# Performance work log

Hardware: AMD Instinct MI355X
Metric: run time of the kernel (lower is better)

## Reference

```python
import jax, jax.numpy as jnp
import numpy as np

N_QUBITS = 14      # must be even (module assert)
IN_CHANNEL = 512   # batch of independent circuits

# PennyLane convention: wire 0 is the most-significant bit of the basis index.

def _mcx_perm(n, c1, c2, t):
    # MultiControlledX with control_values '10': flip target bit t when bit(c1)==1 and bit(c2)==0
    idx = np.arange(2 ** n)
    b1 = (idx >> (n - 1 - c1)) & 1
    b2 = (idx >> (n - 1 - c2)) & 1
    return np.where((b1 == 1) & (b2 == 0), idx ^ (1 << (n - 1 - t)), idx)

_MCX_PERMS = [jnp.asarray(_mcx_perm(N_QUBITS, w, (w + 1) % N_QUBITS, (w + 2) % N_QUBITS))
              for w in range(N_QUBITS)]
# Z-eigenvalue signs per basis state per wire: (2^n, n)
_Z_SIGNS = jnp.asarray(
    np.stack([1.0 - 2.0 * ((np.arange(2 ** N_QUBITS) >> (N_QUBITS - 1 - w)) & 1)
              for w in range(N_QUBITS)], axis=1), dtype=jnp.float32)


def _apply_rx(state, theta, w):
    # RX(theta) = [[cos(t/2), -i sin(t/2)], [-i sin(t/2), cos(t/2)]] on wire w; theta: (B,)
    B = state.shape[0]
    st = state.reshape(B, 2 ** w, 2, -1)
    c = jnp.cos(0.5 * theta)[:, None, None]
    s = (-1j * jnp.sin(0.5 * theta))[:, None, None]
    s0, s1 = st[:, :, 0, :], st[:, :, 1, :]
    out = jnp.stack([c * s0 + s * s1, c * s1 + s * s0], axis=2)
    return out.reshape(B, -1)


def _apply_rz(state, theta, w):
    # RZ(theta) = diag(e^{-i t/2}, e^{+i t/2}) on wire w
    B = state.shape[0]
    st = state.reshape(B, 2 ** w, 2, -1)
    p0 = jnp.exp(-0.5j * theta)[:, None, None]
    p1 = jnp.exp(0.5j * theta)[:, None, None]
    out = jnp.stack([p0 * st[:, :, 0, :], p1 * st[:, :, 1, :]], axis=2)
    return out.reshape(B, -1)


def _apply_isingxx(state, phi, wa, wb):
    a, b = min(wa, wb), max(wa, wb)
    B = state.shape[0]
    st = state.reshape(B, 2 ** a, 2, 2 ** (b - a - 1), 2, -1)
    c = jnp.cos(0.5 * phi)[:, None, None, None]
    s = (-1j * jnp.sin(0.5 * phi))[:, None, None, None]
    s00 = st[:, :, 0, :, 0, :]; s01 = st[:, :, 0, :, 1, :]
    s10 = st[:, :, 1, :, 0, :]; s11 = st[:, :, 1, :, 1, :]
    row0 = jnp.stack([c * s00 + s * s11, c * s01 + s * s10], axis=3)  # (B, 2^a, M, 2, R)
    row1 = jnp.stack([c * s10 + s * s01, c * s11 + s * s00], axis=3)
    return jnp.stack([row0, row1], axis=2).reshape(B, -1)


def _circuit(cp, p):
    n = N_QUBITS
    B = cp.shape[0]
    state = jnp.zeros((B, 2 ** n), dtype=jnp.complex64).at[:, 0].set(1.0)
    for w in range(n):
        state = _apply_rx(state, p[:, 0, w], w)
    for ws in range(n // 2):
        state = _apply_isingxx(state, cp[:, ws], 2 * ws, 2 * ws + 1)
    for w in range(n):
        state = _apply_rz(state, p[:, 1, w], w)
    for ws in range(n // 2):
        wss = 2 * ws + 1
        state = _apply_isingxx(state, cp[:, ws + n // 2], wss, (wss + 1) % n)
    for w in range(n):
        state = _apply_rx(state, p[:, 2, w], w)
    for w in range(n):
        state = state[:, _MCX_PERMS[w]]
    probs = state.real ** 2 + state.imag ** 2  # (B, 2^n)
    return (probs @ _Z_SIGNS).astype(jnp.float32)  # (B, n) = expval PauliZ per wire


def setup_inputs() -> dict:
    key = jax.random.key(0)
    k1, k2 = jax.random.split(key)
    cp = jax.random.uniform(k1, (IN_CHANNEL, N_QUBITS), dtype=jnp.float32) * jnp.pi
    p = jax.random.uniform(k2, (IN_CHANNEL, 3, N_QUBITS), dtype=jnp.float32) * jnp.pi
    return {"cp": cp, "p": p}


def reference(cp, p):
    return _circuit(cp, p)
```

## Files before the change

kernel.cpp:

```cpp
#include <hip/hip_runtime.h>

#define NQ 14
#define NSTATE (1 << NQ)

typedef float  f2  __attribute__((ext_vector_type(2)));
typedef __fp16 h2v __attribute__((ext_vector_type(2)));

#define OFF_BTAB  (NSTATE*4)
#define OFF_RX3   (OFF_BTAB + 28*8)
#define OFF_XX2   (OFF_RX3 + 28*4)
#define OFF_RED   (OFF_XX2 + 14*4)
#define SMEM_BYTES (OFF_RED + 16*NQ*4)

__device__ __forceinline__ f2 cmul(f2 a, f2 b){
    f2 br = {-b.y, b.x};
    return a.x * b + a.y * br;
}

__device__ __forceinline__ void rot2(f2& A, f2& B, float c, float sn){
    f2 a = A, b = B;
    f2 ar = {a.y, -a.x};
    f2 br = {b.y, -b.x};
    A = c * a + sn * br;
    B = c * b + sn * ar;
}

__device__ __forceinline__ h2v pack(f2 v){ return __builtin_amdgcn_cvt_pkrtz(v.x, v.y); }
__device__ __forceinline__ f2  unpack(h2v h){ return (f2){(float)h.x, (float)h.y}; }

__device__ __forceinline__ int slotof(int i){ return i ^ ((i >> 5) & 31); }

__device__ __forceinline__ void gates16(f2 amp[16], float c0, float s0, float c1, float s1,
                                        const float* rc, const float* rs, int w0)
{
    #pragma unroll
    for (int lo = 0; lo < 4; ++lo) { rot2(amp[lo], amp[lo|12], c0, s0); rot2(amp[lo|4], amp[lo|8], c0, s0); }
    #pragma unroll
    for (int hi = 0; hi < 16; hi += 4) { rot2(amp[hi], amp[hi|3], c1, s1); rot2(amp[hi|1], amp[hi|2], c1, s1); }
    #pragma unroll
    for (int j = 0; j < 4; ++j) {
        const int bm = 1 << (3 - j);
        const float c = rc[w0 + j], s = rs[w0 + j];
        #pragma unroll
        for (int L = 0; L < 16; ++L)
            if (!(L & bm)) rot2(amp[L], amp[L | bm], c, s);
    }
}

__global__ void perm_tbl_kernel(unsigned short* __restrict__ tbl)
{
    const int i = blockIdx.x * blockDim.x + threadIdx.x;
    int x = i;
    #pragma unroll
    for (int w = 13; w >= 0; --w) {
        const int p1 = 13 - w;
        const int p2 = 13 - ((w + 1) % NQ);
        const int pt = 13 - ((w + 2) % NQ);
        const int cond = ((x >> p1) & ~(x >> p2)) & 1;
        x ^= cond << pt;
    }
    const int slot = x ^ ((x >> 5) & 31);
    tbl[(i & 1023) * 16 + (i >> 10)] = (unsigned short)slot;
}

__global__ void __launch_bounds__(1024, 8)
qsim_kernel(const float* __restrict__ cp, const float* __restrict__ p,
            const unsigned short* __restrict__ tbl, float* __restrict__ out)
{
    extern __shared__ __align__(16) char smem[];
    h2v* st    = reinterpret_cast<h2v*>(smem);
    f2*  Btab  = reinterpret_cast<f2*>(smem + OFF_BTAB);
    float* rx3c = reinterpret_cast<float*>(smem + OFF_RX3);
    float* rx3s = rx3c + 14;
    float* xx2c = reinterpret_cast<float*>(smem + OFF_XX2);
    float* xx2s = xx2c + 7;
    float* red  = reinterpret_cast<float*>(smem + OFF_RED);

    const int b = blockIdx.x;
    const int t = threadIdx.x;
    const float* pb  = p  + b * 42;
    const float* cpb = cp + b * 14;

    if (t < 7) {
        const int ws = t, wa = 2*ws, wb = 2*ws + 1;
        float sa, ca; sincosf(0.5f * pb[wa], &sa, &ca);
        float sb, cb; sincosf(0.5f * pb[wb], &sb, &cb);
        f2 s00 = {ca*cb, 0.f};
        f2 s01 = {0.f, -ca*sb};
        f2 s10 = {0.f, -sa*cb};
        f2 s11 = {-sa*sb, 0.f};
        float sx, cx; sincosf(0.5f * cpb[ws], &sx, &cx);
        rot2(s00, s11, cx, sx);
        rot2(s01, s10, cx, sx);
        const float ga = 0.5f * pb[14 + wa], gb = 0.5f * pb[14 + wb];
        float sA, cA; sincosf(ga + gb, &sA, &cA);
        float sB, cB; sincosf(gb - ga, &sB, &cB);
        s00 = cmul(s00, (f2){cA, -sA});
        s11 = cmul(s11, (f2){cA,  sA});
        s01 = cmul(s01, (f2){cB,  sB});
        s10 = cmul(s10, (f2){cB, -sB});
        const int k = 6 - ws;
        Btab[k*4+0] = s00; Btab[k*4+1] = s01; Btab[k*4+2] = s10; Btab[k*4+3] = s11;
    } else if (t >= 64 && t < 78) {
        const int w = t - 64;
        float s, c; sincosf(0.5f * pb[28 + w], &s, &c);
        rx3c[w] = c; rx3s[w] = s;
    } else if (t >= 128 && t < 135) {
        const int g = t - 128;
        float s, c; sincosf(0.5f * cpb[7 + g], &s, &c);
        xx2c[g] = c; xx2s[g] = s;
    }
    __syncthreads();

    f2 amp[16];

    {
        const int ibase = (t & 0x1FF) | ((t >> 9) << 13);
        f2 Pc = cmul(cmul(Btab[(ibase & 3)],            Btab[4  + ((ibase >> 2) & 3)]),
                     cmul(Btab[8 + ((ibase >> 4) & 3)], Btab[12 + ((ibase >> 6) & 3)]));
        const int b8  = (ibase >> 8) & 1;
        const int b13 = (ibase >> 13) & 1;
        #pragma unroll
        for (int L = 0; L < 16; ++L) {
            const int c4 = ((L & 1) << 1) | b8;
            const int c5 = (L >> 1) & 3;
            const int c6 = (b13 << 1) | ((L >> 3) & 1);
            amp[L] = cmul(cmul(Pc, Btab[16 + c4]), cmul(Btab[20 + c5], Btab[24 + c6]));
        }
        gates16(amp, xx2c[0], xx2s[0], xx2c[1], xx2s[1], rx3c, rx3s, 1);
        #pragma unroll
        for (int L = 0; L < 16; ++L) st[slotof(ibase | (L << 9))] = pack(amp[L]);
    }
    __syncthreads();

    {
        const int ibase = (t & 31) | ((t >> 5) << 9);
        #pragma unroll
        for (int L = 0; L < 16; ++L) amp[L] = unpack(st[slotof(ibase | (L << 5))]);
        gates16(amp, xx2c[2], xx2s[2], xx2c[3], xx2s[3], rx3c, rx3s, 5);
        #pragma unroll
        for (int L = 0; L < 16; ++L) st[slotof(ibase | (L << 5))] = pack(amp[L]);
    }
    __syncthreads();

    {
        const int ibase = (t & 1) | ((t >> 1) << 5);
        #pragma unroll
        for (int L = 0; L < 16; ++L) amp[L] = unpack(st[slotof(ibase | (L << 1))]);
        gates16(amp, xx2c[4], xx2s[4], xx2c[5], xx2s[5], rx3c, rx3s, 9);
        #pragma unroll
        for (int L = 0; L < 16; ++L) st[slotof(ibase | (L << 1))] = pack(amp[L]);
    }
    __syncthreads();

    {
        const int tb = t << 3;
        #pragma unroll
        for (int L = 0; L < 16; ++L) {
            const int i = tb | (L & 1) | (((L >> 1) & 1) << 13) | (((L >> 2) & 1) << 1) | (((L >> 3) & 1) << 2);
            amp[L] = unpack(st[slotof(i)]);
        }
        {
            const float c = xx2c[6], s = xx2s[6];
            #pragma unroll
            for (int f = 0; f < 16; f += 4) { rot2(amp[f], amp[f|3], c, s); rot2(amp[f|1], amp[f|2], c, s); }
        }
        {
            const float c = rx3c[13], s = rx3s[13];
            #pragma unroll
            for (int L = 0; L < 16; ++L) if (!(L & 1)) rot2(amp[L], amp[L|1], c, s);
        }
        {
            const float c = rx3c[0], s = rx3s[0];
            #pragma unroll
            for (int L = 0; L < 16; ++L) if (!(L & 2)) rot2(amp[L], amp[L|2], c, s);
        }
        #pragma unroll
        for (int L = 0; L < 16; ++L) {
            const int i = tb | (L & 1) | (((L >> 1) & 1) << 13) | (((L >> 2) & 1) << 1) | (((L >> 3) & 1) << 2);
            st[slotof(i)] = pack(amp[L]);
        }
    }
    __syncthreads();

    {
        unsigned off[16];
        {
            const uint4* tp = reinterpret_cast<const uint4*>(tbl + t * 16);
            const uint4 w0 = tp[0], w1 = tp[1];
            off[0]=w0.x&0xffffu; off[1]=w0.x>>16; off[2]=w0.y&0xffffu; off[3]=w0.y>>16;
            off[4]=w0.z&0xffffu; off[5]=w0.z>>16; off[6]=w0.w&0xffffu; off[7]=w0.w>>16;
            off[8]=w1.x&0xffffu; off[9]=w1.x>>16; off[10]=w1.y&0xffffu; off[11]=w1.y>>16;
            off[12]=w1.z&0xffffu; off[13]=w1.z>>16; off[14]=w1.w&0xffffu; off[15]=w1.w>>16;
        }
        float T = 0.f, U0 = 0.f, U1 = 0.f, U2 = 0.f, U3 = 0.f;
        #pragma unroll
        for (int k = 0; k < 16; ++k) {
            const f2 a = unpack(st[off[k]]);
            const float q = fmaf(a.x, a.x, a.y * a.y);
            T += q;
            if (k & 1) U0 += q;
            if (k & 2) U1 += q;
            if (k & 4) U2 += q;
            if (k & 8) U3 += q;
        }
        float s = T;
        float d0, d1, d2, d3, d4, d5;
        {
            float o;
            o = __shfl_xor(s, 1);  d0 = s - o; s += o;
            o = __shfl_xor(d0, 2); d0 += o;
            o = __shfl_xor(s, 2);  d1 = s - o; s += o;
            o = __shfl_xor(d0, 4); d0 += o;
            o = __shfl_xor(d1, 4); d1 += o;
            o = __shfl_xor(s, 4);  d2 = s - o; s += o;
            o = __shfl_xor(d0, 8); d0 += o;
            o = __shfl_xor(d1, 8); d1 += o;
            o = __shfl_xor(d2, 8); d2 += o;
            o = __shfl_xor(s, 8);  d3 = s - o; s += o;
            o = __shfl_xor(d0, 16); d0 += o;
            o = __shfl_xor(d1, 16); d1 += o;
            o = __shfl_xor(d2, 16); d2 += o;
            o = __shfl_xor(d3, 16); d3 += o;
            o = __shfl_xor(s, 16);  d4 = s - o; s += o;
            o = __shfl_xor(d0, 32); d0 += o;
            o = __shfl_xor(d1, 32); d1 += o;
            o = __shfl_xor(d2, 32); d2 += o;
            o = __shfl_xor(d3, 32); d3 += o;
            o = __shfl_xor(d4, 32); d4 += o;
            o = __shfl_xor(s, 32);  d5 = s - o; s += o;
        }
        #pragma unroll
        for (int m = 1; m < 64; m <<= 1) {
            U0 += __shfl_xor(U0, m);
            U1 += __shfl_xor(U1, m);
            U2 += __shfl_xor(U2, m);
            U3 += __shfl_xor(U3, m);
        }
        if ((t & 63) == 0) {
            const int v = t >> 6;
            float* r = red + v * NQ;
            r[0]  = s - 2.f * U3;
            r[1]  = s - 2.f * U2;
            r[2]  = s - 2.f * U1;
            r[3]  = s - 2.f * U0;
            r[4]  = (v & 8) ? -s : s;
            r[5]  = (v & 4) ? -s : s;
            r[6]  = (v & 2) ? -s : s;
            r[7]  = (v & 1) ? -s : s;
            r[8]  = d5;
            r[9]  = d4;
            r[10] = d3;
            r[11] = d2;
            r[12] = d1;
            r[13] = d0;
        }
    }
    __syncthreads();
    if (t < NQ) {
        float ssum = 0.f;
        #pragma unroll
        for (int wv = 0; wv < 16; ++wv) ssum += red[wv * NQ + t];
        out[b * NQ + t] = ssum;
    }
}

extern "C" void kernel_launch(void* const* d_in, const int* in_sizes, int n_in,
                              void* d_out, int out_size, void* d_ws, size_t ws_size,
                              hipStream_t stream)
{
    (void)n_in; (void)out_size; (void)ws_size;
    const float* cp = (const float*)d_in[0];
    const float* p  = (const float*)d_in[1];
    float* out = (float*)d_out;
    unsigned short* tbl = (unsigned short*)d_ws;
    const int B = in_sizes[0] / NQ;

    perm_tbl_kernel<<<NSTATE / 256, 256, 0, stream>>>(tbl);

    (void)hipFuncSetAttribute(reinterpret_cast<const void*>(qsim_kernel),
                              hipFuncAttributeMaxDynamicSharedMemorySize, SMEM_BYTES);
    qsim_kernel<<<B, 1024, SMEM_BYTES, stream>>>(cp, p, tbl, out);
}
```

Before: 89.28 us.

## Scatter final stage through forward MCX permutation into padded rows, read contiguously

Replaces the gather through the inverse MCX permutation in the reduction with a forward scatter. The last gate stage now writes each amplitude directly to its permuted position in a padded layout (row stride 72 bytes). This lets each thread read its 16 output amplitudes as 8 contiguous 4-half vectors and drops the separate store-then-gather pass. The table kernel now computes the forward permutation indexed by thread and register, and the shared-memory footprint grows by 8 KB for padding. An extra barrier is added before the scatter, and the reduction's wire-to-output mapping is reordered to match the new layout.

```diff
diff --git a/kernel.cpp b/kernel.cpp
--- a/kernel.cpp
+++ b/kernel.cpp
@@ -5,8 +5,9 @@
 
 typedef float  f2  __attribute__((ext_vector_type(2)));
 typedef __fp16 h2v __attribute__((ext_vector_type(2)));
-
-#define OFF_BTAB  (NSTATE*4)
+typedef __fp16 h4v __attribute__((ext_vector_type(4)));
+
+#define OFF_BTAB  (NSTATE*4 + 1024*8)
 #define OFF_RX3   (OFF_BTAB + 28*8)
 #define OFF_XX2   (OFF_RX3 + 28*4)
 #define OFF_RED   (OFF_XX2 + 14*4)
@@ -47,25 +48,26 @@
     }
 }
 
-__global__ void perm_tbl_kernel(unsigned short* __restrict__ tbl)
-{
-    const int i = blockIdx.x * blockDim.x + threadIdx.x;
-    int x = i;
-    #pragma unroll
-    for (int w = 13; w >= 0; --w) {
+__global__ void perm_tbl_kernel(unsigned short* __restrict__ tblD)
+{
+    const int j = blockIdx.x * blockDim.x + threadIdx.x;
+    int x = j;
+    #pragma unroll
+    for (int w = 0; w < NQ; ++w) {
         const int p1 = 13 - w;
         const int p2 = 13 - ((w + 1) % NQ);
         const int pt = 13 - ((w + 2) % NQ);
         const int cond = ((x >> p1) & ~(x >> p2)) & 1;
         x ^= cond << pt;
     }
-    const int slot = x ^ ((x >> 5) & 31);
-    tbl[(i & 1023) * 16 + (i >> 10)] = (unsigned short)slot;
+    const int t = (j >> 3) & 0x3FF;
+    const int L = (j & 1) | (((j >> 13) & 1) << 1) | (((j >> 1) & 1) << 2) | (((j >> 2) & 1) << 3);
+    tblD[t * 16 + L] = (unsigned short)x;
 }
 
 __global__ void __launch_bounds__(1024, 8)
 qsim_kernel(const float* __restrict__ cp, const float* __restrict__ p,
-            const unsigned short* __restrict__ tbl, float* __restrict__ out)
+            const unsigned short* __restrict__ tblD, float* __restrict__ out)
 {
     extern __shared__ __align__(16) char smem[];
     h2v* st    = reinterpret_cast<h2v*>(smem);
@@ -154,6 +156,9 @@
     __syncthreads();
 
     {
+        const uint4* tp = reinterpret_cast<const uint4*>(tblD + t * 16);
+        const uint4 w0 = tp[0], w1 = tp[1];
+
         const int tb = t << 3;
         #pragma unroll
         for (int L = 0; L < 16; ++L) {
@@ -175,34 +180,37 @@
             #pragma unroll
             for (int L = 0; L < 16; ++L) if (!(L & 2)) rot2(amp[L], amp[L|2], c, s);
         }
+        __syncthreads();
+
+        unsigned d[16];
+        d[0]=w0.x&0xffffu; d[1]=w0.x>>16; d[2]=w0.y&0xffffu; d[3]=w0.y>>16;
+        d[4]=w0.z&0xffffu; d[5]=w0.z>>16; d[6]=w0.w&0xffffu; d[7]=w0.w>>16;
+        d[8]=w1.x&0xffffu; d[9]=w1.x>>16; d[10]=w1.y&0xffffu; d[11]=w1.y>>16;
+        d[12]=w1.z&0xffffu; d[13]=w1.z>>16; d[14]=w1.w&0xffffu; d[15]=w1.w>>16;
         #pragma unroll
         for (int L = 0; L < 16; ++L) {
-            const int i = tb | (L & 1) | (((L >> 1) & 1) << 13) | (((L >> 2) & 1) << 1) | (((L >> 3) & 1) << 2);
-            st[slotof(i)] = pack(amp[L]);
-        }
-    }
-    __syncthreads();
-
-    {
-        unsigned off[16];
-        {
-            const uint4* tp = reinterpret_cast<const uint4*>(tbl + t * 16);
-            const uint4 w0 = tp[0], w1 = tp[1];
-            off[0]=w0.x&0xffffu; off[1]=w0.x>>16; off[2]=w0.y&0xffffu; off[3]=w0.y>>16;
-            off[4]=w0.z&0xffffu; off[5]=w0.z>>16; off[6]=w0.w&0xffffu; off[7]=w0.w>>16;
-            off[8]=w1.x&0xffffu; off[9]=w1.x>>16; off[10]=w1.y&0xffffu; off[11]=w1.y>>16;
-            off[12]=w1.z&0xffffu; off[13]=w1.z>>16; off[14]=w1.w&0xffffu; off[15]=w1.w>>16;
-        }
+            const unsigned f = d[L];
+            st[f + ((f >> 4) << 1)] = pack(amp[L]);
+        }
+    }
+    __syncthreads();
+
+    {
+        const h4v* row = reinterpret_cast<const h4v*>(smem + t * 72);
         float T = 0.f, U0 = 0.f, U1 = 0.f, U2 = 0.f, U3 = 0.f;
         #pragma unroll
-        for (int k = 0; k < 16; ++k) {
-            const f2 a = unpack(st[off[k]]);
-            const float q = fmaf(a.x, a.x, a.y * a.y);
-            T += q;
-            if (k & 1) U0 += q;
-            if (k & 2) U1 += q;
-            if (k & 4) U2 += q;
-            if (k & 8) U3 += q;
+        for (int m = 0; m < 8; ++m) {
+            const h4v h = row[m];
+            const float a0 = (float)h.x, a1 = (float)h.y;
+            const float b0 = (float)h.z, b1 = (float)h.w;
+            const float q0 = fmaf(a0, a0, a1 * a1);
+            const float q1 = fmaf(b0, b0, b1 * b1);
+            const float qs = q0 + q1;
+            T += qs;
+            U0 += q1;
+            if (m & 1) U1 += qs;
+            if (m & 2) U2 += qs;
+            if (m & 4) U3 += qs;
         }
         float s = T;
         float d0, d1, d2, d3, d4, d5;
@@ -240,20 +248,20 @@
         if ((t & 63) == 0) {
             const int v = t >> 6;
             float* r = red + v * NQ;
-            r[0]  = s - 2.f * U3;
-            r[1]  = s - 2.f * U2;
-            r[2]  = s - 2.f * U1;
-            r[3]  = s - 2.f * U0;
-            r[4]  = (v & 8) ? -s : s;
-            r[5]  = (v & 4) ? -s : s;
-            r[6]  = (v & 2) ? -s : s;
-            r[7]  = (v & 1) ? -s : s;
-            r[8]  = d5;
-            r[9]  = d4;
-            r[10] = d3;
-            r[11] = d2;
-            r[12] = d1;
-            r[13] = d0;
+            r[0]  = (v & 8) ? -s : s;
+            r[1]  = (v & 4) ? -s : s;
+            r[2]  = (v & 2) ? -s : s;
+            r[3]  = (v & 1) ? -s : s;
+            r[4]  = d5;
+            r[5]  = d4;
+            r[6]  = d3;
+            r[7]  = d2;
+            r[8]  = d1;
+            r[9]  = d0;
+            r[10] = s - 2.f * U3;
+            r[11] = s - 2.f * U2;
+            r[12] = s - 2.f * U1;
+            r[13] = s - 2.f * U0;
         }
     }
     __syncthreads();
@@ -273,12 +281,12 @@
     const float* cp = (const float*)d_in[0];
     const float* p  = (const float*)d_in[1];
     float* out = (float*)d_out;
-    unsigned short* tbl = (unsigned short*)d_ws;
+    unsigned short* tblD = (unsigned short*)d_ws;
     const int B = in_sizes[0] / NQ;
 
-    perm_tbl_kernel<<<NSTATE / 256, 256, 0, stream>>>(tbl);
+    perm_tbl_kernel<<<NSTATE / 256, 256, 0, stream>>>(tblD);
 
     (void)hipFuncSetAttribute(reinterpret_cast<const void*>(qsim_kernel),
                               hipFuncAttributeMaxDynamicSharedMemorySize, SMEM_BYTES);
-    qsim_kernel<<<B, 1024, SMEM_BYTES, stream>>>(cp, p, tbl, out);
-}
+    qsim_kernel<<<B, 1024, SMEM_BYTES, stream>>>(cp, p, tblD, out);
+}
```

After: 87.51 us. 2.0% less time.

## Use 256 threads with 64 amplitudes each, fusing gate phases and permuting on store

Applied to the files above, without the earlier changes.

Blocks shrink from 1024 to 256 threads, and each thread now holds 64 amplitudes in registers. This lets each shared-memory pass apply six wires' worth of gates, which cuts the number of shared-memory round trips and barriers from five to three. The MCX permutation is now done as a scatter when writing to shared memory, using a padded row layout so the final Pauli-Z reduction reads contiguous rows. rot2 is rewritten with packed-FP32 inline assembly (v_pk_mul/v_pk_fma). The costs are heavy register pressure from 64 complex amplitudes per thread, which may limit occupancy or cause spills, plus more complex index bookkeeping.

```diff
diff --git a/kernel.cpp b/kernel.cpp
--- a/kernel.cpp
+++ b/kernel.cpp
@@ -2,70 +2,78 @@
 
 #define NQ 14
 #define NSTATE (1 << NQ)
+#define NT 256
+#define AMPS 64
 
 typedef float  f2  __attribute__((ext_vector_type(2)));
 typedef __fp16 h2v __attribute__((ext_vector_type(2)));
 
-#define OFF_BTAB  (NSTATE*4)
+#define N_H2 16640
+#define OFF_BTAB  (N_H2*4)
 #define OFF_RX3   (OFF_BTAB + 28*8)
 #define OFF_XX2   (OFF_RX3 + 28*4)
 #define OFF_RED   (OFF_XX2 + 14*4)
-#define SMEM_BYTES (OFF_RED + 16*NQ*4)
+#define SMEM_BYTES (OFF_RED + 4*NQ*4)
 
 __device__ __forceinline__ f2 cmul(f2 a, f2 b){
     f2 br = {-b.y, b.x};
     return a.x * b + a.y * br;
 }
 
-__device__ __forceinline__ void rot2(f2& A, f2& B, float c, float sn){
-    f2 a = A, b = B;
-    f2 ar = {a.y, -a.x};
-    f2 br = {b.y, -b.x};
-    A = c * a + sn * br;
-    B = c * b + sn * ar;
+__device__ __forceinline__ f2 pkswz(f2 ss, f2 y){
+    f2 t;
+    asm("v_pk_mul_f32 %0, %1, %2 op_sel:[0,1] op_sel_hi:[1,0] neg_hi:[0,1]"
+        : "=v"(t) : "v"(ss), "v"(y));
+    return t;
+}
+__device__ __forceinline__ f2 pkfma(f2 a, f2 b, f2 c){
+    f2 d;
+    asm("v_pk_fma_f32 %0, %1, %2, %3" : "=v"(d) : "v"(a), "v"(b), "v"(c));
+    return d;
+}
+__device__ __forceinline__ void rot2(f2& A, f2& B, f2 cc, f2 ss){
+    f2 tA = pkswz(ss, B);
+    f2 tB = pkswz(ss, A);
+    A = pkfma(cc, A, tA);
+    B = pkfma(cc, B, tB);
 }
 
 __device__ __forceinline__ h2v pack(f2 v){ return __builtin_amdgcn_cvt_pkrtz(v.x, v.y); }
 __device__ __forceinline__ f2  unpack(h2v h){ return (f2){(float)h.x, (float)h.y}; }
 
-__device__ __forceinline__ int slotof(int i){ return i ^ ((i >> 5) & 31); }
-
-__device__ __forceinline__ void gates16(f2 amp[16], float c0, float s0, float c1, float s1,
-                                        const float* rc, const float* rs, int w0)
-{
+template<int P, int M>
+__device__ __forceinline__ void applyXX(f2* amp, f2 cc, f2 ss){
     #pragma unroll
-    for (int lo = 0; lo < 4; ++lo) { rot2(amp[lo], amp[lo|12], c0, s0); rot2(amp[lo|4], amp[lo|8], c0, s0); }
+    for (int L = 0; L < AMPS; ++L)
+        if (!((L >> P) & 1)) rot2(amp[L], amp[L ^ M], cc, ss);
+}
+template<int R>
+__device__ __forceinline__ void applyRX(f2* amp, f2 cc, f2 ss){
     #pragma unroll
-    for (int hi = 0; hi < 16; hi += 4) { rot2(amp[hi], amp[hi|3], c1, s1); rot2(amp[hi|1], amp[hi|2], c1, s1); }
-    #pragma unroll
-    for (int j = 0; j < 4; ++j) {
-        const int bm = 1 << (3 - j);
-        const float c = rc[w0 + j], s = rs[w0 + j];
-        #pragma unroll
-        for (int L = 0; L < 16; ++L)
-            if (!(L & bm)) rot2(amp[L], amp[L | bm], c, s);
-    }
+    for (int L = 0; L < AMPS; ++L)
+        if (!((L >> R) & 1)) rot2(amp[L], amp[L | (1 << R)], cc, ss);
 }
 
 __global__ void perm_tbl_kernel(unsigned short* __restrict__ tbl)
 {
-    const int i = blockIdx.x * blockDim.x + threadIdx.x;
-    int x = i;
+    const int j = blockIdx.x * blockDim.x + threadIdx.x;
+    int x = j;
     #pragma unroll
-    for (int w = 13; w >= 0; --w) {
+    for (int w = 0; w < NQ; ++w) {
         const int p1 = 13 - w;
         const int p2 = 13 - ((w + 1) % NQ);
         const int pt = 13 - ((w + 2) % NQ);
         const int cond = ((x >> p1) & ~(x >> p2)) & 1;
         x ^= cond << pt;
     }
-    const int slot = x ^ ((x >> 5) & 31);
-    tbl[(i & 1023) * 16 + (i >> 10)] = (unsigned short)slot;
-}
-
-__global__ void __launch_bounds__(1024, 8)
+    const int t = ((j >> 1) & 15) | (((j >> 7) & 1) << 4) | (j & 0x60) | (((j >> 8) & 1) << 7);
+    const int L = (j & 1) | (((j >> 13) & 1) << 1) | (((j >> 9) & 15) << 2);
+    tbl[(L >> 3) * 2048 + t * 8 + (L & 7)] = (unsigned short)x;
+}
+
+__global__ void __launch_bounds__(NT, 2)
 qsim_kernel(const float* __restrict__ cp, const float* __restrict__ p,
-            const unsigned short* __restrict__ tbl, float* __restrict__ out)
+            const unsigned short* __restrict__ tblD, float* __restrict__ out)
 {
     extern __shared__ __align__(16) char smem[];
     h2v* st    = reinterpret_cast<h2v*>(smem);
@@ -90,8 +98,8 @@
         f2 s10 = {0.f, -sa*cb};
         f2 s11 = {-sa*sb, 0.f};
         float sx, cx; sincosf(0.5f * cpb[ws], &sx, &cx);
-        rot2(s00, s11, cx, sx);
-        rot2(s01, s10, cx, sx);
+        rot2(s00, s11, (f2){cx,cx}, (f2){sx,sx});
+        rot2(s01, s10, (f2){cx,cx}, (f2){sx,sx});
         const float ga = 0.5f * pb[14 + wa], gb = 0.5f * pb[14 + wb];
         float sA, cA; sincosf(ga + gb, &sA, &cA);
         float sB, cB; sincosf(gb - ga, &sB, &cB);
@@ -112,98 +120,127 @@
     }
     __syncthreads();
 
-    f2 amp[16];
+    f2 amp[AMPS];
+    f2 cc, ss;
+    #define LOADXX(g) do { float c_ = xx2c[g], s_ = xx2s[g]; cc = (f2){c_,c_}; ss = (f2){s_,s_}; } while (0)
+    #define LOADRX(w) do { float c_ = rx3c[w], s_ = rx3s[w]; cc = (f2){c_,c_}; ss = (f2){s_,s_}; } while (0)
+
 
     {
-        const int ibase = (t & 0x1FF) | ((t >> 9) << 13);
-        f2 Pc = cmul(cmul(Btab[(ibase & 3)],            Btab[4  + ((ibase >> 2) & 3)]),
-                     cmul(Btab[8 + ((ibase >> 4) & 3)], Btab[12 + ((ibase >> 6) & 3)]));
-        const int b8  = (ibase >> 8) & 1;
-        const int b13 = (ibase >> 13) & 1;
-        #pragma unroll
-        for (int L = 0; L < 16; ++L) {
-            const int c4 = ((L & 1) << 1) | b8;
-            const int c5 = (L >> 1) & 3;
-            const int c6 = (b13 << 1) | ((L >> 3) & 1);
-            amp[L] = cmul(cmul(Pc, Btab[16 + c4]), cmul(Btab[20 + c5], Btab[24 + c6]));
-        }
-        gates16(amp, xx2c[0], xx2s[0], xx2c[1], xx2s[1], rx3c, rx3s, 1);
-        #pragma unroll
-        for (int L = 0; L < 16; ++L) st[slotof(ibase | (L << 9))] = pack(amp[L]);
+        const int t6 = (t >> 6) & 1, t7 = t >> 7;
+        f2 Pc = cmul(cmul(Btab[t & 3], Btab[4 + ((t >> 2) & 3)]), Btab[8 + ((t >> 4) & 3)]);
+        f2 P3a0 = cmul(Pc, Btab[12 + t6]);
+        f2 P3a1 = cmul(Pc, Btab[12 + 2 + t6]);
+        f2 G00 = cmul(P3a0, Btab[24 + (t7 << 1)]);
+        f2 G01 = cmul(P3a0, Btab[24 + (t7 << 1) + 1]);
+        f2 G10 = cmul(P3a1, Btab[24 + (t7 << 1)]);
+        f2 G11 = cmul(P3a1, Btab[24 + (t7 << 1) + 1]);
+        #pragma unroll
+        for (int m = 0; m < 16; ++m) {
+            f2 H = cmul(Btab[16 + (m & 3)], Btab[20 + (m >> 2)]);
+            amp[(m << 1)]          = cmul(G00, H);
+            amp[(m << 1) | 1]      = cmul(G10, H);
+            amp[32 | (m << 1)]     = cmul(G01, H);
+            amp[32 | (m << 1) | 1] = cmul(G11, H);
+        }
+        LOADXX(0); applyXX<5, 0x30>(amp, cc, ss);
+        LOADXX(1); applyXX<3, 0x0C>(amp, cc, ss);
+        LOADXX(2); applyXX<1, 0x03>(amp, cc, ss);
+        LOADRX(1); applyRX<5>(amp, cc, ss);
+        LOADRX(2); applyRX<4>(amp, cc, ss);
+        LOADRX(3); applyRX<3>(amp, cc, ss);
+        LOADRX(4); applyRX<2>(amp, cc, ss);
+        LOADRX(5); applyRX<1>(amp, cc, ss);
+        LOADRX(6); applyRX<0>(amp, cc, ss);
+        const int jbase = (t7 << 13) | (t & 127);
+        #pragma unroll
+        for (int L = 0; L < AMPS; ++L) {
+            const int j = jbase | (L << 7);
+            st[j ^ ((j >> 7) & 127)] = pack(amp[L]);
+        }
     }
     __syncthreads();
 
     {
-        const int ibase = (t & 31) | ((t >> 5) << 9);
-        #pragma unroll
-        for (int L = 0; L < 16; ++L) amp[L] = unpack(st[slotof(ibase | (L << 5))]);
-        gates16(amp, xx2c[2], xx2s[2], xx2c[3], xx2s[3], rx3c, rx3s, 5);
-        #pragma unroll
-        for (int L = 0; L < 16; ++L) st[slotof(ibase | (L << 5))] = pack(amp[L]);
+        const int t0 = t & 1, thi = t >> 1;
+        const int hi7 = thi << 7;
+        #pragma unroll
+        for (int L = 0; L < AMPS; ++L)
+            amp[L] = unpack(st[hi7 | (((L << 1) | t0) ^ thi)]);
+        LOADXX(3); applyXX<5, 0x30>(amp, cc, ss);
+        LOADXX(4); applyXX<3, 0x0C>(amp, cc, ss);
+        LOADXX(5); applyXX<1, 0x03>(amp, cc, ss);
+        LOADRX(7);  applyRX<5>(amp, cc, ss);
+        LOADRX(8);  applyRX<4>(amp, cc, ss);
+        LOADRX(9);  applyRX<3>(amp, cc, ss);
+        LOADRX(10); applyRX<2>(amp, cc, ss);
+        LOADRX(11); applyRX<1>(amp, cc, ss);
+        LOADRX(12); applyRX<0>(amp, cc, ss);
+        #pragma unroll
+        for (int L = 0; L < AMPS; ++L)
+            st[hi7 | (((L << 1) | t0) ^ thi)] = pack(amp[L]);
     }
     __syncthreads();
 
     {
-        const int ibase = (t & 1) | ((t >> 1) << 5);
-        #pragma unroll
-        for (int L = 0; L < 16; ++L) amp[L] = unpack(st[slotof(ibase | (L << 1))]);
-        gates16(amp, xx2c[4], xx2s[4], xx2c[5], xx2s[5], rx3c, rx3s, 9);
-        #pragma unroll
-        for (int L = 0; L < 16; ++L) st[slotof(ibase | (L << 1))] = pack(amp[L]);
+        uint4 tv[8];
+        const uint4* tq = reinterpret_cast<const uint4*>(tblD);
+        #pragma unroll
+        for (int g = 0; g < 8; ++g) tv[g] = tq[g * 256 + t];
+
+        const int tbase = ((t & 15) << 1) | (t & 0x60) | (((t >> 4) & 1) << 7) | (((t >> 7) & 1) << 8);
+        #pragma unroll
+        for (int L = 0; L < AMPS; ++L) {
+            const int j = tbase | (L & 1) | (((L >> 1) & 1) << 13) | (((L >> 2) & 15) << 9);
+            amp[L] = unpack(st[j ^ ((j >> 7) & 127)]);
+        }
+        LOADXX(6);  applyXX<0, 0x03>(amp, cc, ss);
+        LOADRX(13); applyRX<0>(amp, cc, ss);
+        LOADRX(0);  applyRX<1>(amp, cc, ss);
+        __syncthreads();
+        #pragma unroll
+        for (int L = 0; L < AMPS; ++L) {
+            const unsigned comp = (L & 4) ? ((L & 2) ? tv[L >> 3].w : tv[L >> 3].z)
+                                          : ((L & 2) ? tv[L >> 3].y : tv[L >> 3].x);
+            const unsigned f = (L & 1) ? (comp >> 16) : (comp & 0xffffu);
+            st[f + (f >> 6)] = pack(amp[L]);
+        }
     }
     __syncthreads();
 
     {
-        const int tb = t << 3;
-        #pragma unroll
-        for (int L = 0; L < 16; ++L) {
-            const int i = tb | (L & 1) | (((L >> 1) & 1) << 13) | (((L >> 2) & 1) << 1) | (((L >> 3) & 1) << 2);
-            amp[L] = unpack(st[slotof(i)]);
-        }
+        const h2v* erow = st + t * 65;
+        float U0, U1 = 0.f, U2 = 0.f, U4, U5, T;
+        float C[8];
+        float u0acc = 0.f;
+        #pragma unroll
+        for (int ch = 0; ch < 8; ++ch) {
+            float q[8];
+            #pragma unroll
+            for (int e = 0; e < 8; ++e) {
+                const f2 a = unpack(erow[ch * 8 + e]);
+                q[e] = fmaf(a.x, a.x, a.y * a.y);
+            }
+            const float p0 = q[0] + q[1], p1 = q[2] + q[3], p2 = q[4] + q[5], p3 = q[6] + q[7];
+            u0acc += (q[1] + q[3]) + (q[5] + q[7]);
+            U1 += p1 + p3;
+            const float s01 = p0 + p1, s23 = p2 + p3;
+            U2 += s23;
+            C[ch] = s01 + s23;
+        }
+        U0 = u0acc;
         {
-            const float c = xx2c[6], s = xx2s[6];
-            #pragma unroll
-            for (int f = 0; f < 16; f += 4) { rot2(amp[f], amp[f|3], c, s); rot2(amp[f|1], amp[f|2], c, s); }
-        }
-        {
-            const float c = rx3c[13], s = rx3s[13];
-            #pragma unroll
-            for (int L = 0; L < 16; ++L) if (!(L & 1)) rot2(amp[L], amp[L|1], c, s);
-        }
-        {
-            const float c = rx3c[0], s = rx3s[0];
-            #pragma unroll
-            for (int L = 0; L < 16; ++L) if (!(L & 2)) rot2(amp[L], amp[L|2], c, s);
-        }
-        #pragma unroll
-        for (int L = 0; L < 16; ++L) {
-            const int i = tb | (L & 1) | (((L >> 1) & 1) << 13) | (((L >> 2) & 1) << 1) | (((L >> 3) & 1) << 2);
-            st[slotof(i)] = pack(amp[L]);
-        }
-    }
-    __syncthreads();
-
-    {
-        unsigned off[16];
-        {
-            const uint4* tp = reinterpret_cast<const uint4*>(tbl + t * 16);
-            const uint4 w0 = tp[0], w1 = tp[1];
-            off[0]=w0.x&0xffffu; off[1]=w0.x>>16; off[2]=w0.y&0xffffu; off[3]=w0.y>>16;
-            off[4]=w0.z&0xffffu; off[5]=w0.z>>16; off[6]=w0.w&0xffffu; off[7]=w0.w>>16;
-            off[8]=w1.x&0xffffu; off[9]=w1.x>>16; off[10]=w1.y&0xffffu; off[11]=w1.y>>16;
-            off[12]=w1.z&0xffffu; off[13]=w1.z>>16; off[14]=w1.w&0xffffu; off[15]=w1.w>>16;
-        }
-        float T = 0.f, U0 = 0.f, U1 = 0.f, U2 = 0.f, U3 = 0.f;
-        #pragma unroll
-        for (int k = 0; k < 16; ++k) {
-            const f2 a = unpack(st[off[k]]);
-            const float q = fmaf(a.x, a.x, a.y * a.y);
-            T += q;
-            if (k & 1) U0 += q;
-            if (k & 2) U1 += q;
-            if (k & 4) U2 += q;
-            if (k & 8) U3 += q;
-        }
+            const float P0 = C[0] + C[1], P1 = C[2] + C[3], P2 = C[4] + C[5], P3v = C[6] + C[7];
+            const float U3v = (C[1] + C[3]) + (C[5] + C[7]);
+            U4 = P1 + P3v;
+            const float Q0 = P0 + P1, Q1 = P2 + P3v;
+            U5 = Q1;
+            T = Q0 + Q1;
+            U2 += 0.f;
+            C[0] = U3v;
+        }
+        const float U3 = C[0];
+
         float s = T;
         float d0, d1, d2, d3, d4, d5;
         {
@@ -230,39 +267,41 @@
             o = __shfl_xor(d4, 32); d4 += o;
             o = __shfl_xor(s, 32);  d5 = s - o; s += o;
         }
+        float V0 = U0, V1 = U1, V2 = U2, V3 = U3, V4 = U4, V5 = U5;
         #pragma unroll
         for (int m = 1; m < 64; m <<= 1) {
-            U0 += __shfl_xor(U0, m);
-            U1 += __shfl_xor(U1, m);
-            U2 += __shfl_xor(U2, m);
-            U3 += __shfl_xor(U3, m);
+            V0 += __shfl_xor(V0, m);
+            V1 += __shfl_xor(V1, m);
+            V2 += __shfl_xor(V2, m);
+            V3 += __shfl_xor(V3, m);
+            V4 += __shfl_xor(V4, m);
+            V5 += __shfl_xor(V5, m);
         }
         if ((t & 63) == 0) {
-            const int v = t >> 6;
-            float* r = red + v * NQ;
-            r[0]  = s - 2.f * U3;
-            r[1]  = s - 2.f * U2;
-            r[2]  = s - 2.f * U1;
-            r[3]  = s - 2.f * U0;
-            r[4]  = (v & 8) ? -s : s;
-            r[5]  = (v & 4) ? -s : s;
-            r[6]  = (v & 2) ? -s : s;
-            r[7]  = (v & 1) ? -s : s;
-            r[8]  = d5;
-            r[9]  = d4;
-            r[10] = d3;
-            r[11] = d2;
-            r[12] = d1;
-            r[13] = d0;
+            const int wv = t >> 6;
+            float* r = red + wv * NQ;
+            r[0]  = (wv & 2) ? -s : s;
+            r[1]  = (wv & 1) ? -s : s;
+            r[2]  = d5;
+            r[3]  = d4;
+            r[4]  = d3;
+            r[5]  = d2;
+            r[6]  = d1;
+            r[7]  = d0;
+            r[8]  = s - 2.f * V5;
+            r[9]  = s - 2.f * V4;
+            r[10] = s - 2.f * V3;
+            r[11] = s - 2.f * V2;
+            r[12] = s - 2.f * V1;
+            r[13] = s - 2.f * V0;
         }
     }
     __syncthreads();
     if (t < NQ) {
-        float ssum = 0.f;
-        #pragma unroll
-        for (int wv = 0; wv < 16; ++wv) ssum += red[wv * NQ + t];
-        out[b * NQ + t] = ssum;
-    }
+        out[b * NQ + t] = (red[t] + red[NQ + t]) + (red[2 * NQ + t] + red[3 * NQ + t]);
+    }
+    #undef LOADXX
+    #undef LOADRX
 }
 
 extern "C" void kernel_launch(void* const* d_in, const int* in_sizes, int n_in,
@@ -280,5 +319,5 @@
 
     (void)hipFuncSetAttribute(reinterpret_cast<const void*>(qsim_kernel),
                               hipFuncAttributeMaxDynamicSharedMemorySize, SMEM_BYTES);
-    qsim_kernel<<<B, 1024, SMEM_BYTES, stream>>>(cp, p, tbl, out);
-}
+    qsim_kernel<<<B, NT, SMEM_BYTES, stream>>>(cp, p, tbl, out);
+}
```

After: 79.35 us. -11.1%, faster.
